# Optimization experiments

Hardware: AMD Instinct MI355X
Metric: run time of the kernel (lower is better)

Reference implementation:

```python
import jax, jax.numpy as jnp
import numpy as np

B, CIN, COUT, H, W = 16, 96, 96, 96, 96
K = 3   # hidden_kernels (conv), odd -> same padding
A = 3   # attn_kernels, odd -> stride-1 unfold preserves H*W positions


def _conv(x, w, p):
    # NCHW conv with symmetric padding p, stride 1, no bias
    return jax.lax.conv_general_dilated(
        x, w, window_strides=(1, 1), padding=[(p, p), (p, p)],
        dimension_numbers=("NCHW", "OIHW", "NCHW"))


def _unfold_nonoverlap(y, a):
    # torch nn.Unfold(a, stride=a): [B,C,H,W] -> [B, C*a*a, L], channel-major (c,kh,kw)
    b, c, h, w = y.shape
    hb, wb = h // a, w // a
    y = y.reshape(b, c, hb, a, wb, a).transpose(0, 1, 3, 5, 2, 4)
    return y.reshape(b, c * a * a, hb * wb)


def _unfold_stride1(y, a):
    # torch nn.Unfold(a, padding=a//2): [B,C,H,W] -> [B, C*a*a, H*W]
    b, c, h, w = y.shape
    p = a // 2
    yp = jnp.pad(y, ((0, 0), (0, 0), (p, p), (p, p)))
    # small fixed a*a loop (9 shifts), channel-major (c,kh,kw) ordering
    patches = jnp.stack([yp[:, :, i:i + h, j:j + w]
                         for i in range(a) for j in range(a)], axis=2)
    return patches.reshape(b, c * a * a, h * w)


def setup_inputs() -> dict:
    key = jax.random.key(0)
    kx, k1, k2, k3 = jax.random.split(key, 4)
    x = jax.random.normal(kx, (B, CIN, H, W), dtype=jnp.float32)
    W1 = jax.random.normal(k1, (COUT, CIN, K, K), dtype=jnp.float32) * 0.05
    W2 = jax.random.normal(k2, (COUT, CIN, K, K), dtype=jnp.float32) * 0.05
    W3 = jax.random.normal(k3, (COUT, CIN, K, K), dtype=jnp.float32) * 0.05
    return {"x": x, "W1": W1, "W2": W2, "W3": W3}


def reference(x, W1, W2, W3):
    a, c, p = A, COUT, K // 2
    b = x.shape[0]
    y1 = _unfold_nonoverlap(_conv(x, W1, p), a)   # [B, C*a^2, L]
    y2 = _unfold_nonoverlap(_conv(x, W2, p), a)   # [B, C*a^2, L]
    L = y1.shape[-1]
    y1 = y1.reshape(b, c, a * a, L).transpose(0, 2, 1, 3)  # [B, a^2, C, L]
    y2 = y2.reshape(b, c, a * a, L).transpose(0, 2, 3, 1)  # [B, a^2, L, C]
    attn = jnp.einsum("bkcl,bkld->bkcd", y1, y2)           # [B, a^2, C, C]
    # torch: transpose(1,3).flatten(2) -> [B, C, C*a^2], then scale + softmax(dim=2)
    attn = attn.transpose(0, 3, 2, 1).reshape(b, c, c * a * a)
    attn = jax.nn.softmax(attn / np.float32(np.sqrt(c * a * a)), axis=2)
    v = _unfold_stride1(_conv(x, W3, p), a)        # [B, C*a^2, H*W]
    out = jnp.einsum("bcm,bml->bcl", attn, v)      # [B, C, H*W]
    return out.reshape(b, c, H, W)
```

## Files before the change

kernel.cpp:

```cpp
#include <hip/hip_runtime.h>
#include <math.h>
#include <stdint.h>

constexpr int BB  = 16;
constexpr int CH  = 96;
constexpr int HH  = 96;
constexpr int WW  = 96;
constexpr int HWI = HH * WW;
constexpr int CHW = CH * HWI;
constexpr int IMG = BB * CHW;
constexpr int ATT = BB * CH * CH * 9;
constexpr int WPK = 27 * 6 * 64 * 8;

typedef short short8 __attribute__((ext_vector_type(8)));
typedef float floatx4 __attribute__((ext_vector_type(4)));

__device__ __forceinline__ ushort f2bf(float f) {
  union { float f; unsigned u; } v; v.f = f;
  unsigned r = (v.u + 0x7fffu + ((v.u >> 16) & 1u)) >> 16;
  return (ushort)r;
}
__device__ __forceinline__ float bf2f(ushort h) {
  union { float f; unsigned u; } v; v.u = ((unsigned)h) << 16;
  return v.f;
}
__device__ __forceinline__ uint packhl(float v) {
  const ushort h = f2bf(v);
  const ushort l = f2bf(v - bf2f(h));
  return (uint)h | ((uint)l << 16);
}

__device__ __forceinline__ void gl_lds_b128(const void* g, void* s) {
  auto gp = (const __attribute__((address_space(1))) void*)(uintptr_t)g;
  auto sp = (__attribute__((address_space(3))) void*)(uintptr_t)s;
  __builtin_amdgcn_global_load_lds(gp, sp, 16, 0, 0);
}

__global__ __launch_bounds__(256) void xcast(
    const float* __restrict__ X, ushort* __restrict__ Xn)
{
  const int b  = blockIdx.y;
  const int p0 = blockIdx.x * 256;
  const int tid = threadIdx.x;
  __shared__ ushort T[256 * 104];

  const float* xb = X + (size_t)b * CHW + p0;
#pragma unroll 8
  for (int c = 0; c < 96; c += 2) {
    const ushort h0 = f2bf(xb[(size_t)c * HWI + tid]);
    const ushort h1 = f2bf(xb[(size_t)(c + 1) * HWI + tid]);
    *(uint*)(&T[tid * 104 + c]) = (uint)h0 | ((uint)h1 << 16);
  }
  __syncthreads();

  ushort* ob = Xn + (size_t)b * CHW + (size_t)p0 * 96;
#pragma unroll
  for (int it = 0; it < 12; ++it) {
    const int idx = it * 256 + tid;
    const int pix = (idx * 2731) >> 15;
    const int c8  = idx - pix * 12;
    *(short8*)(ob + pix * 96 + c8 * 8) = *(const short8*)(&T[pix * 104 + c8 * 8]);
  }
}

__global__ __launch_bounds__(256) void prepack(
    const float* __restrict__ src, ushort* __restrict__ dst)
{
  const int g = blockIdx.y;
  const int p = blockIdx.x * 256 + threadIdx.x;
  const float* s = src + (size_t)g * WPK;
  ushort* d = dst + (size_t)g * WPK;
  const int j    = p & 7;
  const int lane = (p >> 3) & 63;
  const int rest = p >> 9;
  const int mt = rest % 6;
  const int kc = rest / 6;
  const int m  = mt * 16 + (lane & 15);
  const int k  = kc * 32 + (lane >> 4) * 8 + j;
  const int ci = k % 96;
  const int o  = k / 96;
  d[p] = f2bf(s[m * 864 + ci * 9 + o]);
}

template<int OUTM>
__global__ __launch_bounds__(512, 2) void conv_nb(
    const ushort* __restrict__ Xn,
    const ushort* __restrict__ Wpk,
    void* __restrict__ Yv, int wbstride)
{
  const int b    = blockIdx.y;
  const int tile = blockIdx.x;
  const int ty0  = (tile / 6) * 12;
  const int tx0  = (tile % 6) * 16;
  const int tid  = threadIdx.x;
  const int lane = tid & 63;
  const int w8   = tid >> 6;
  const int wr   = w8 >> 1;
  const int half = w8 & 1;
  const int nc   = lane & 15;
  const int q    = lane >> 4;

  __shared__ __attribute__((aligned(16))) ushort Xs[252 * 104];
  __shared__ __attribute__((aligned(16))) ushort Ws[9 * 3072];

  const ushort* wp = Wpk + (size_t)b * wbstride;

  for (int i = 0; i < 7; ++i) {
    const int pp = w8 + 8 * i;
    if (pp < 54)
      gl_lds_b128(wp + (size_t)pp * 512 + lane * 8,
                  (ushort*)Ws + __builtin_amdgcn_readfirstlane(pp * 512));
  }

  const ushort* xb = Xn + (size_t)b * CHW;
  for (int it = 0; it < 6; ++it) {
    const int idx = it * 512 + tid;
    if (idx < 3024) {
      const int pix = (idx * 2731) >> 15;
      const int c8  = idx - pix * 12;
      const int ly  = (pix * 57) >> 10;
      const int lx  = pix - ly * 18;
      const int gy  = ty0 - 1 + ly, gx = tx0 - 1 + lx;
      short8 v = {0, 0, 0, 0, 0, 0, 0, 0};
      if (((unsigned)gy < 96u) & ((unsigned)gx < 96u))
        v = *(const short8*)(xb + ((size_t)gy * WW + gx) * 96 + c8 * 8);
      *(short8*)(&Xs[pix * 104 + c8 * 8]) = v;
    }
  }
  __syncthreads();

  floatx4 acc[3][3];
#pragma unroll
  for (int mtl = 0; mtl < 3; ++mtl)
#pragma unroll
    for (int t = 0; t < 3; ++t)
#pragma unroll
      for (int r = 0; r < 4; ++r) acc[mtl][t][r] = 0.f;

  for (int g = 0; g < 3; ++g) {
    if (g) {
      __syncthreads();
      for (int i = 0; i < 7; ++i) {
        const int pp = w8 + 8 * i;
        if (pp < 54)
          gl_lds_b128(wp + (size_t)(g * 54 + pp) * 512 + lane * 8,
                      (ushort*)Ws + __builtin_amdgcn_readfirstlane(pp * 512));
      }
      __syncthreads();
    }

#pragma unroll
    for (int oo = 0; oo < 3; ++oo) {
#pragma unroll
      for (int cc = 0; cc < 3; ++cc) {
        const int kcL = oo * 3 + cc;
        const int pc  = nc + oo;
        const int cib = cc * 32 + q * 8;

        short8 bfr[3];
#pragma unroll
        for (int t = 0; t < 3; ++t) {
          const int pix = (3 * wr + t + g) * 18 + pc;
          bfr[t] = *(const short8*)(&Xs[pix * 104 + cib]);
        }

        const ushort* ap = (const ushort*)Ws + kcL * 3072 + (half * 3) * 512
                         + lane * 8;
#pragma unroll
        for (int mtl = 0; mtl < 3; ++mtl) {
          const short8 af = *(const short8*)(ap + mtl * 512);
#pragma unroll
          for (int t = 0; t < 3; ++t)
            acc[mtl][t] = __builtin_amdgcn_mfma_f32_16x16x32_bf16(
                af, bfr[t], acc[mtl][t], 0, 0, 0);
        }
      }
    }
  }

#pragma unroll
  for (int mtl = 0; mtl < 3; ++mtl)
#pragma unroll
    for (int t = 0; t < 3; ++t) {
      const int yy = ty0 + 3 * wr + t;
      const int xx = tx0 + nc;
#pragma unroll
      for (int r = 0; r < 4; ++r) {
        const int co = (half * 3 + mtl) * 16 + q * 4 + r;
        if constexpr (OUTM == 0) {
          const int cx = xx / 3;
          const int kw = xx - 3 * cx;
          const int kk = t * 3 + kw;
          const int cp = (ty0 / 3 + wr) * 32 + cx;
          ((uint*)Yv)[(((size_t)b * 9 + kk) * CH + co) * 1024 + cp] =
              packhl(acc[mtl][t][r]);
        } else if constexpr (OUTM == 1) {
          ((ushort*)Yv + (size_t)b * CHW)[((size_t)yy * WW + xx) * 96 + co] =
              f2bf(acc[mtl][t][r]);
        } else {
          ((float*)Yv + (size_t)b * CHW)[(size_t)co * HWI + yy * WW + xx] =
              acc[mtl][t][r];
        }
      }
    }
}

__global__ __launch_bounds__(256) void attn_mfma(
    const uint* __restrict__ Y1, const uint* __restrict__ Y2,
    float* __restrict__ P0, float* __restrict__ P1,
    float* __restrict__ P2, float* __restrict__ P3)
{
  const int bi = blockIdx.x;
  const int b  = bi / 36;
  const int r9 = bi % 36;
  const int k  = r9 >> 2;
  const int qd = r9 & 3;
  const int tid  = threadIdx.x;
  const int lane = tid & 63;
  const int wv   = tid >> 6;

  __shared__ ushort Ah[96 * 72], Al[96 * 72], Bh[96 * 72], Bl[96 * 72];

  const uint* y1b = Y1 + ((size_t)(b * 9 + k) * CH) * 1024;
  const uint* y2b = Y2 + ((size_t)(b * 9 + k) * CH) * 1024;

  const int mg2 = wv >> 1;
  const int ng2 = wv & 1;
  const int cn = lane & 15;
  const int q  = lane >> 4;

  floatx4 acc[3][3];
#pragma unroll
  for (int i = 0; i < 3; ++i)
#pragma unroll
    for (int j = 0; j < 3; ++j)
#pragma unroll
      for (int r = 0; r < 4; ++r) acc[i][j][r] = 0.f;

  const int sj4  = tid & 15;
  const int sg16 = tid >> 4;

  for (int ss = 0; ss < 4; ++ss) {
    const int s = qd * 4 + ss;
    __syncthreads();
#pragma unroll
    for (int cg = 0; cg < 6; ++cg) {
      const int c = cg * 16 + sg16;
      const size_t goff = (size_t)c * 1024 + s * 64 + sj4 * 4;
      const uint4 u1 = *(const uint4*)(y1b + goff);
      const uint4 u2 = *(const uint4*)(y2b + goff);
      const int lbase = c * 72 + sj4 * 4;
      uint2 w;
      w.x = (u1.x & 0xffffu) | (u1.y << 16);
      w.y = (u1.z & 0xffffu) | (u1.w << 16);
      *(uint2*)(&Ah[lbase]) = w;
      w.x = (u1.x >> 16) | (u1.y & 0xffff0000u);
      w.y = (u1.z >> 16) | (u1.w & 0xffff0000u);
      *(uint2*)(&Al[lbase]) = w;
      w.x = (u2.x & 0xffffu) | (u2.y << 16);
      w.y = (u2.z & 0xffffu) | (u2.w << 16);
      *(uint2*)(&Bh[lbase]) = w;
      w.x = (u2.x >> 16) | (u2.y & 0xffff0000u);
      w.y = (u2.z >> 16) | (u2.w & 0xffff0000u);
      *(uint2*)(&Bl[lbase]) = w;
    }
    __syncthreads();

#pragma unroll
    for (int kc = 0; kc < 2; ++kc) {
      short8 ah[3], al[3], bh[3], bl[3];
#pragma unroll
      for (int t = 0; t < 3; ++t) {
        const int offA = (mg2 * 48 + t * 16 + cn) * 72 + kc * 32 + q * 8;
        ah[t] = *(const short8*)(&Ah[offA]);
        al[t] = *(const short8*)(&Al[offA]);
        const int offB = (ng2 * 48 + t * 16 + cn) * 72 + kc * 32 + q * 8;
        bh[t] = *(const short8*)(&Bh[offB]);
        bl[t] = *(const short8*)(&Bl[offB]);
      }
#pragma unroll
      for (int i = 0; i < 3; ++i)
#pragma unroll
        for (int j = 0; j < 3; ++j) {
          acc[i][j] = __builtin_amdgcn_mfma_f32_16x16x32_bf16(
              ah[i], bh[j], acc[i][j], 0, 0, 0);
          acc[i][j] = __builtin_amdgcn_mfma_f32_16x16x32_bf16(
              ah[i], bl[j], acc[i][j], 0, 0, 0);
          acc[i][j] = __builtin_amdgcn_mfma_f32_16x16x32_bf16(
              al[i], bh[j], acc[i][j], 0, 0, 0);
        }
    }
  }

  float* P = (qd == 0) ? P0 : (qd == 1) ? P1 : (qd == 2) ? P2 : P3;
#pragma unroll
  for (int i = 0; i < 3; ++i)
#pragma unroll
    for (int j = 0; j < 3; ++j)
#pragma unroll
      for (int r = 0; r < 4; ++r) {
        const int c = mg2 * 48 + i * 16 + q * 4 + r;
        const int d = ng2 * 48 + j * 16 + cn;
        P[((size_t)(b * CH + d) * CH + c) * 9 + k] = acc[i][j][r];
      }
}

__global__ __launch_bounds__(256) void softmax_k(
    const float* __restrict__ P0, const float* __restrict__ P1,
    const float* __restrict__ P2, const float* __restrict__ P3,
    float* __restrict__ attnW)
{
  const int bd = blockIdx.x;
  const size_t base = (size_t)bd * 864;
  float* dst = attnW + base;
  const float rs = 0.0340216824f;
  const int tid = threadIdx.x;

  const size_t i0 = base + tid;
  float v0 = P0[i0] + P1[i0] + P2[i0] + P3[i0];
  float v1 = P0[i0 + 256] + P1[i0 + 256] + P2[i0 + 256] + P3[i0 + 256];
  float v2 = P0[i0 + 512] + P1[i0 + 512] + P2[i0 + 512] + P3[i0 + 512];
  float v3 = (tid < 96)
      ? (P0[i0 + 768] + P1[i0 + 768] + P2[i0 + 768] + P3[i0 + 768])
      : -3.0e38f;

  float mx = fmaxf(fmaxf(v0, v1), fmaxf(v2, v3));

  __shared__ float red[256];
  red[tid] = mx;
  __syncthreads();
#pragma unroll
  for (int s = 128; s > 0; s >>= 1) {
    if (tid < s) red[tid] = fmaxf(red[tid], red[tid + s]);
    __syncthreads();
  }
  mx = red[0];
  __syncthreads();

  const float e0 = expf((v0 - mx) * rs);
  const float e1 = expf((v1 - mx) * rs);
  const float e2 = expf((v2 - mx) * rs);
  const float e3 = (tid < 96) ? expf((v3 - mx) * rs) : 0.f;

  red[tid] = e0 + e1 + e2 + e3;
  __syncthreads();
#pragma unroll
  for (int s = 128; s > 0; s >>= 1) {
    if (tid < s) red[tid] += red[tid + s];
    __syncthreads();
  }
  const float inv = 1.f / red[0];

  dst[tid]       = e0 * inv;
  dst[tid + 256] = e1 * inv;
  dst[tid + 512] = e2 * inv;
  if (tid < 96) dst[tid + 768] = e3 * inv;
}

extern "C" void kernel_launch(void* const* d_in, const int* in_sizes, int n_in,
                              void* d_out, int out_size, void* d_ws, size_t ws_size,
                              hipStream_t stream)
{
  const float* x  = (const float*)d_in[0];
  const float* W1 = (const float*)d_in[1];
  const float* W2 = (const float*)d_in[2];
  const float* W3 = (const float*)d_in[3];

  float* ws    = (float*)d_ws;
  uint*  Y1    = (uint*)ws;
  uint*  Y2    = Y1 + (size_t)IMG;
  float* attnT = (float*)(Y2 + (size_t)IMG);
  float* attnW = attnT + ATT;
  ushort* pk   = (ushort*)(attnW + ATT);
  ushort* pkW1 = pk;
  ushort* pkW2 = pk + WPK;
  ushort* pkW3 = pk + 2 * (size_t)WPK;
  ushort* pkAW = pk + 3 * (size_t)WPK;
  ushort* Xn   = pkAW + 16 * (size_t)WPK;
  float* Pd2   = (float*)d_out;
  float* Pd3   = Pd2 + ATT;
  ushort* Y3n  = (ushort*)Y1;

  const dim3 cgrid(48, BB);

  xcast    <<<dim3(36, BB), 256, 0, stream>>>(x, Xn);

  prepack  <<<dim3(324, 1),  256, 0, stream>>>(W1, pkW1);
  prepack  <<<dim3(324, 1),  256, 0, stream>>>(W2, pkW2);
  prepack  <<<dim3(324, 1),  256, 0, stream>>>(W3, pkW3);

  conv_nb<0><<<cgrid, 512, 0, stream>>>(Xn, pkW1, Y1, 0);
  conv_nb<0><<<cgrid, 512, 0, stream>>>(Xn, pkW2, Y2, 0);

  attn_mfma<<<BB * 9 * 4, 256, 0, stream>>>(Y1, Y2, attnT, attnW, Pd2, Pd3);
  softmax_k<<<BB * CH, 256, 0, stream>>>(attnT, attnW, Pd2, Pd3, attnW);

  prepack  <<<dim3(324, BB), 256, 0, stream>>>(attnW, pkAW);

  conv_nb<1><<<cgrid, 512, 0, stream>>>(Xn, pkW3, Y3n, 0);
  conv_nb<2><<<cgrid, 512, 0, stream>>>(Y3n, pkAW, d_out, WPK);
}
```

Baseline: 359.9 us.

## Stream conv weights directly from global into registers instead of staging in LDS

The conv kernel no longer stages weight chunks into shared memory through async global-to-LDS loads with barriers between the three groups. Each wave now loads its A-fragments straight from global memory into registers, prefetching the next chunk's fragments one step ahead inside a flattened 27-step loop. With the 55 KB weight buffer gone, launch bounds are raised to allow 4 blocks per CU. The intent is to cut barriers and LDS pressure and raise occupancy, at the cost of repeated global (L2) weight reads across blocks and possible register pressure under the tighter bound.

```diff
diff --git a/kernel.cpp b/kernel.cpp
--- a/kernel.cpp
+++ b/kernel.cpp
@@ -28,12 +28,6 @@
   const ushort h = f2bf(v);
   const ushort l = f2bf(v - bf2f(h));
   return (uint)h | ((uint)l << 16);
-}
-
-__device__ __forceinline__ void gl_lds_b128(const void* g, void* s) {
-  auto gp = (const __attribute__((address_space(1))) void*)(uintptr_t)g;
-  auto sp = (__attribute__((address_space(3))) void*)(uintptr_t)s;
-  __builtin_amdgcn_global_load_lds(gp, sp, 16, 0, 0);
 }
 
 __global__ __launch_bounds__(256) void xcast(
@@ -83,7 +77,7 @@
 }
 
 template<int OUTM>
-__global__ __launch_bounds__(512, 2) void conv_nb(
+__global__ __launch_bounds__(512, 4) void conv_nb(
     const ushort* __restrict__ Xn,
     const ushort* __restrict__ Wpk,
     void* __restrict__ Yv, int wbstride)
@@ -101,16 +95,9 @@
   const int q    = lane >> 4;
 
   __shared__ __attribute__((aligned(16))) ushort Xs[252 * 104];
-  __shared__ __attribute__((aligned(16))) ushort Ws[9 * 3072];
-
-  const ushort* wp = Wpk + (size_t)b * wbstride;
-
-  for (int i = 0; i < 7; ++i) {
-    const int pp = w8 + 8 * i;
-    if (pp < 54)
-      gl_lds_b128(wp + (size_t)pp * 512 + lane * 8,
-                  (ushort*)Ws + __builtin_amdgcn_readfirstlane(pp * 512));
-  }
+
+  const ushort* wph = Wpk + (size_t)b * wbstride + (size_t)(half * 3) * 512
+                    + lane * 8;
 
   const ushort* xb = Xn + (size_t)b * CHW;
   for (int it = 0; it < 6; ++it) {
@@ -127,7 +114,11 @@
       *(short8*)(&Xs[pix * 104 + c8 * 8]) = v;
     }
   }
-  __syncthreads();
+
+  short8 af[3];
+#pragma unroll
+  for (int m = 0; m < 3; ++m)
+    af[m] = *(const short8*)(wph + m * 512);
 
   floatx4 acc[3][3];
 #pragma unroll
@@ -137,45 +128,39 @@
 #pragma unroll
       for (int r = 0; r < 4; ++r) acc[mtl][t][r] = 0.f;
 
-  for (int g = 0; g < 3; ++g) {
-    if (g) {
-      __syncthreads();
-      for (int i = 0; i < 7; ++i) {
-        const int pp = w8 + 8 * i;
-        if (pp < 54)
-          gl_lds_b128(wp + (size_t)(g * 54 + pp) * 512 + lane * 8,
-                      (ushort*)Ws + __builtin_amdgcn_readfirstlane(pp * 512));
-      }
-      __syncthreads();
-    }
-
-#pragma unroll
-    for (int oo = 0; oo < 3; ++oo) {
-#pragma unroll
-      for (int cc = 0; cc < 3; ++cc) {
-        const int kcL = oo * 3 + cc;
-        const int pc  = nc + oo;
-        const int cib = cc * 32 + q * 8;
-
-        short8 bfr[3];
-#pragma unroll
-        for (int t = 0; t < 3; ++t) {
-          const int pix = (3 * wr + t + g) * 18 + pc;
-          bfr[t] = *(const short8*)(&Xs[pix * 104 + cib]);
-        }
-
-        const ushort* ap = (const ushort*)Ws + kcL * 3072 + (half * 3) * 512
-                         + lane * 8;
-#pragma unroll
-        for (int mtl = 0; mtl < 3; ++mtl) {
-          const short8 af = *(const short8*)(ap + mtl * 512);
-#pragma unroll
-          for (int t = 0; t < 3; ++t)
-            acc[mtl][t] = __builtin_amdgcn_mfma_f32_16x16x32_bf16(
-                af, bfr[t], acc[mtl][t], 0, 0, 0);
-        }
-      }
-    }
+  __syncthreads();
+
+#pragma unroll
+  for (int ch = 0; ch < 27; ++ch) {
+    short8 afn[3];
+    if (ch < 26) {
+#pragma unroll
+      for (int m = 0; m < 3; ++m)
+        afn[m] = *(const short8*)(wph + (size_t)(ch + 1) * 3072 + m * 512);
+    }
+
+    const int o  = ch / 3;
+    const int cc = ch - o * 3;
+    const int dy = o / 3, dx = o - dy * 3;
+    const int pc  = nc + dx;
+    const int cib = cc * 32 + q * 8;
+
+    short8 bfr[3];
+#pragma unroll
+    for (int t = 0; t < 3; ++t) {
+      const int pix = (3 * wr + t + dy) * 18 + pc;
+      bfr[t] = *(const short8*)(&Xs[pix * 104 + cib]);
+    }
+
+#pragma unroll
+    for (int mtl = 0; mtl < 3; ++mtl)
+#pragma unroll
+      for (int t = 0; t < 3; ++t)
+        acc[mtl][t] = __builtin_amdgcn_mfma_f32_16x16x32_bf16(
+            af[mtl], bfr[t], acc[mtl][t], 0, 0, 0);
+
+#pragma unroll
+    for (int m = 0; m < 3; ++m) af[m] = afn[m];
   }
 
 #pragma unroll
```

New measurement: 458.8 us. 27.5% more time.
